# Kernel tuning notes

Measured on AMD Instinct MI355X. Metric: run time of the kernel, lower is better.

The kernel has to match this reference:

```python
import jax, jax.numpy as jnp
import numpy as np

B, N, C, H = 1, 2048, 1024, 16


def setup_inputs() -> dict:
    key = jax.random.key(0)
    ks = jax.random.split(key, 8)
    scale = 1.0 / np.sqrt(C)
    d = {"x": jax.random.normal(ks[0], (B, N, C), dtype=jnp.float32)}
    for i, name in enumerate(["q1", "q2", "k1", "k2", "v", "out"]):
        d[f"W_{name}"] = jax.random.normal(ks[1 + i], (C, C), dtype=jnp.float32) * scale
        d[f"b_{name}"] = jnp.zeros((C,), dtype=jnp.float32)
    d["ln_g"] = jnp.ones((C,), dtype=jnp.float32)
    d["ln_b"] = jnp.zeros((C,), dtype=jnp.float32)
    return d


def reference(x, W_q1, b_q1, W_q2, b_q2, W_k1, b_k1, W_k2, b_k2,
              W_v, b_v, W_out, b_out, ln_g, ln_b):
    Bx, Nx, Cx = x.shape
    hd = Cx // H  # head_dim

    def proj(W, b):
        # ResidualMLP with num_layers=-1 and in_dim==out_dim: x + Linear(x)
        return x + x @ W + b

    def split_heads(z):
        return z.reshape(Bx, Nx, H, hd).transpose(0, 2, 1, 3)  # b h n d

    # kernel='identity', norm_q=norm_k=False -> raw projections
    q1 = split_heads(proj(W_q1, b_q1))
    q2 = split_heads(proj(W_q2, b_q2))
    k1 = split_heads(proj(W_k1, b_k1))
    k2 = split_heads(proj(W_k2, b_k2))
    v = split_heads(proj(W_v, b_v))

    # triple attention: elementwise product of the two Gram matrices, then
    # row-normalized (flash-style softmax; kernel also returns lse which the
    # module discards: `_, out = self.attn(...)`)
    s = jnp.einsum('bhnd,bhmd->bhnm', q1, k1) * jnp.einsum('bhnd,bhmd->bhnm', q2, k2)
    p = jax.nn.softmax(s, axis=-1)
    o = jnp.einsum('bhnm,bhmd->bhnd', p, v)

    o = o.transpose(0, 2, 1, 3).reshape(Bx, Nx, Cx)  # b n (h d)

    # LayerNorm (eps=1e-5, torch default)
    mu = o.mean(axis=-1, keepdims=True)
    var = ((o - mu) ** 2).mean(axis=-1, keepdims=True)
    o = (o - mu) / jnp.sqrt(var + 1e-5) * ln_g + ln_b

    return o @ W_out + b_out
```

## Files before the change

### kernel.cpp

```cpp
#include <hip/hip_runtime.h>
#include <hip/hip_bf16.h>
#include <stdint.h>


#define N_SEQ 2048
#define CDIM  1024
#define NHEAD 16
#define HDIM  64

typedef __attribute__((ext_vector_type(8))) short bfrag;
typedef __attribute__((ext_vector_type(4))) float f4;
typedef __attribute__((ext_vector_type(16))) float f16v;
typedef unsigned short u16;

#define MFMA16(a, b, c) __builtin_amdgcn_mfma_f32_16x16x32_bf16((a), (b), (c), 0, 0, 0)
#define MFMA32(a, b, c) __builtin_amdgcn_mfma_f32_32x32x16_bf16((a), (b), (c), 0, 0, 0)

__device__ __forceinline__ float bf2f(u16 u) {
  union { unsigned int i; float f; } c; c.i = ((unsigned int)u) << 16; return c.f;
}
__device__ __forceinline__ u16 f2bf(float f) {
  union { float f; unsigned int i; } c; c.f = f;
  unsigned int i = c.i;
  return (u16)((i + 0x7FFFu + ((i >> 16) & 1u)) >> 16);
}
__device__ __forceinline__ unsigned int pk2(float lo, float hi) {
  __hip_bfloat162 b = __float22bfloat162_rn(make_float2(lo, hi));
  unsigned int u;
  __builtin_memcpy(&u, &b, 4);
  return u;
}

__device__ __forceinline__ void gld16(const void* g, void* lds) {
  __builtin_amdgcn_global_load_lds(
      (const __attribute__((address_space(1))) void*)g,
      (__attribute__((address_space(3))) void*)lds, 16, 0, 0);
}

__global__ __launch_bounds__(256) void k_split_x(
    const float* __restrict__ x, u16* __restrict__ xh, u16* __restrict__ xl) {
  int i = (blockIdx.x * 256 + threadIdx.x) * 4;
  float4 v = *(const float4*)(x + i);
  float vv[4] = {v.x, v.y, v.z, v.w};
  ushort4 h, l;
  u16 hh[4], ll[4];
#pragma unroll
  for (int j = 0; j < 4; j++) {
    hh[j] = f2bf(vv[j]);
    ll[j] = f2bf(vv[j] - bf2f(hh[j]));
  }
  h.x = hh[0]; h.y = hh[1]; h.z = hh[2]; h.w = hh[3];
  l.x = ll[0]; l.y = ll[1]; l.z = ll[2]; l.w = ll[3];
  *(ushort4*)(xh + i) = h;
  *(ushort4*)(xl + i) = l;
}

__global__ __launch_bounds__(256) void k_wsplit(
    const float* __restrict__ W0, const float* __restrict__ W1,
    const float* __restrict__ W2, const float* __restrict__ W3,
    const float* __restrict__ W4, const float* __restrict__ W5,
    u16* __restrict__ wth, u16* __restrict__ wtl) {
  __shared__ float tile[64][65];
  int wz = blockIdx.z;
  const float* W = wz == 0 ? W0 : wz == 1 ? W1 : wz == 2 ? W2 : wz == 3 ? W3 : wz == 4 ? W4 : W5;
  int kb = blockIdx.x * 64, nb = blockIdx.y * 64;
  int t = threadIdx.x;
  int r0 = t >> 4, c0 = (t & 15) * 4;
#pragma unroll
  for (int i = 0; i < 4; i++) {
    int r = r0 + i * 16;
    float4 v = *(const float4*)(W + (size_t)(kb + r) * CDIM + nb + c0);
    tile[r][c0 + 0] = v.x; tile[r][c0 + 1] = v.y; tile[r][c0 + 2] = v.z; tile[r][c0 + 3] = v.w;
  }
  __syncthreads();
#pragma unroll
  for (int i = 0; i < 4; i++) {
    int wn = (t >> 4) + i * 16;
    int wk = (t & 15) * 4;
    ushort4 h, l;
    u16 hh[4], ll[4];
#pragma unroll
    for (int j = 0; j < 4; j++) {
      float v = tile[wk + j][wn];
      hh[j] = f2bf(v);
      ll[j] = f2bf(v - bf2f(hh[j]));
    }
    h.x = hh[0]; h.y = hh[1]; h.z = hh[2]; h.w = hh[3];
    l.x = ll[0]; l.y = ll[1]; l.z = ll[2]; l.w = ll[3];
    size_t off = ((size_t)wz * CDIM + nb + wn) * CDIM + kb + wk;
    *(ushort4*)(wth + off) = h;
    if (wz < 4) *(ushort4*)(wtl + off) = l;
  }
}

__global__ __launch_bounds__(256, 2) void k_proj(
    const u16* __restrict__ xh, const u16* __restrict__ xl,
    const u16* __restrict__ wth, const u16* __restrict__ wtl,
    const float* __restrict__ x,
    const float* __restrict__ b0, const float* __restrict__ b1,
    const float* __restrict__ b2, const float* __restrict__ b3,
    const float* __restrict__ b4,
    u16* __restrict__ qh, u16* __restrict__ ql, u16* __restrict__ vT) {
  __shared__ u16 sAh[128 * 64];
  __shared__ u16 sAl[128 * 64];
  __shared__ u16 sBh[128 * 64];
  __shared__ u16 sBl[128 * 64];
  int t = threadIdx.x;
  int w = blockIdx.x >> 3;
  int n0 = (blockIdx.x & 7) * 128;
  int m0 = blockIdx.y * 128;
  int lane = t & 63, wid = t >> 6;
  int wm = (wid >> 1) * 64, wn = (wid & 1) * 64;
  int lr = lane & 15, lg = lane >> 4;
  const bool split = (w < 4);

  f4 acc[4][4];
#pragma unroll
  for (int i = 0; i < 4; i++)
#pragma unroll
    for (int j = 0; j < 4; j++) acc[i][j] = (f4)0.0f;

  const u16* wbh = wth + (size_t)w * CDIM * CDIM;
  const u16* wbl = wtl + (size_t)w * CDIM * CDIM;

  int srow = t >> 3;
  int scolsw = (((t & 7) ^ ((t >> 3) & 7)) * 8);
  int soff = srow * 64 + (t & 7) * 8;

  for (int kt = 0; kt < CDIM; kt += 64) {
#pragma unroll
    for (int c = 0; c < 4; c++) {
      gld16(xh + (size_t)(m0 + srow + c * 32) * CDIM + kt + scolsw, sAh + soff + c * 2048);
      gld16(wbh + (size_t)(n0 + srow + c * 32) * CDIM + kt + scolsw, sBh + soff + c * 2048);
      if (split) {
        gld16(xl + (size_t)(m0 + srow + c * 32) * CDIM + kt + scolsw, sAl + soff + c * 2048);
        gld16(wbl + (size_t)(n0 + srow + c * 32) * CDIM + kt + scolsw, sBl + soff + c * 2048);
      }
    }
    __syncthreads();
#pragma unroll
    for (int kk = 0; kk < 2; kk++) {
      int cc = (((kk * 4 + lg) ^ (lr & 7))) * 8;
      bfrag afh[4], bvh[4];
#pragma unroll
      for (int mi = 0; mi < 4; mi++)
        afh[mi] = *(const bfrag*)(sAh + (wm + mi * 16 + lr) * 64 + cc);
#pragma unroll
      for (int ni = 0; ni < 4; ni++)
        bvh[ni] = *(const bfrag*)(sBh + (wn + ni * 16 + lr) * 64 + cc);
#pragma unroll
      for (int mi = 0; mi < 4; mi++)
#pragma unroll
        for (int ni = 0; ni < 4; ni++)
          acc[mi][ni] = MFMA16(afh[mi], bvh[ni], acc[mi][ni]);
      if (split) {
        bfrag afl[4], bvl[4];
#pragma unroll
        for (int mi = 0; mi < 4; mi++)
          afl[mi] = *(const bfrag*)(sAl + (wm + mi * 16 + lr) * 64 + cc);
#pragma unroll
        for (int ni = 0; ni < 4; ni++)
          bvl[ni] = *(const bfrag*)(sBl + (wn + ni * 16 + lr) * 64 + cc);
#pragma unroll
        for (int mi = 0; mi < 4; mi++)
#pragma unroll
          for (int ni = 0; ni < 4; ni++) {
            acc[mi][ni] = MFMA16(afh[mi], bvl[ni], acc[mi][ni]);
            acc[mi][ni] = MFMA16(afl[mi], bvh[ni], acc[mi][ni]);
          }
      }
    }
    __syncthreads();
  }

  const float* bias = w == 0 ? b0 : w == 1 ? b1 : w == 2 ? b2 : w == 3 ? b3 : b4;
#pragma unroll
  for (int mi = 0; mi < 4; mi++) {
#pragma unroll
    for (int ni = 0; ni < 4; ni++) {
      int col = n0 + wn + ni * 16 + lr;
      int rowb = m0 + wm + mi * 16 + lg * 4;
      float vv[4];
#pragma unroll
      for (int r = 0; r < 4; r++)
        vv[r] = acc[mi][ni][r] + x[(size_t)(rowb + r) * CDIM + col] + bias[col];
      if (split) {
#pragma unroll
        for (int r = 0; r < 4; r++) {
          u16 h = f2bf(vv[r]);
          u16 l = f2bf(vv[r] - bf2f(h));
          qh[((size_t)w * N_SEQ + rowb + r) * CDIM + col] = h;
          ql[((size_t)w * N_SEQ + rowb + r) * CDIM + col] = l;
        }
      } else {
        ushort4 pv;
        pv.x = f2bf(vv[0]); pv.y = f2bf(vv[1]); pv.z = f2bf(vv[2]); pv.w = f2bf(vv[3]);
        *(ushort4*)(vT + (size_t)col * N_SEQ + rowb) = pv;
      }
    }
  }
}

__global__ __launch_bounds__(256, 2) void k_attn(
    const u16* __restrict__ qkh, const u16* __restrict__ qkl,
    const u16* __restrict__ vT, u16* __restrict__ O0, u16* __restrict__ O1,
    float2* __restrict__ ml) {
  __shared__ u16 sbuf[2][32 * 512];
  int bid = blockIdx.x;
  int khalf = bid >> 8;
  int inner = bid & 255;
  int vb = (inner & 7) * 32 + (inner >> 3);
  int h = vb >> 4;
  int qb = (vb & 15) * 128;
  int t = threadIdx.x, lane = t & 63, wv = t >> 6;
  int l31 = lane & 31, hi5 = lane >> 5;
  const size_t NC = (size_t)N_SEQ * CDIM;
  const int hoff = h * HDIM;
  const int k0 = khalf * (N_SEQ / 2);
  u16* Op = khalf ? O1 : O0;

  int qrow = qb + wv * 32 + l31;
  bfrag q1h[4], q1l[4], q2h[4], q2l[4];
#pragma unroll
  for (int ks = 0; ks < 4; ks++) {
    size_t off = (size_t)qrow * CDIM + hoff + ks * 16 + hi5 * 8;
    q1h[ks] = *(const bfrag*)(qkh + off);
    q1l[ks] = *(const bfrag*)(qkl + off);
    q2h[ks] = *(const bfrag*)(qkh + NC + off);
    q2l[ks] = *(const bfrag*)(qkl + NC + off);
  }

  const u16* kb = ((wv & 1) ? qkl : qkh) + (size_t)(2 + (wv >> 1)) * NC;

  float mrun = -1e30f, lrun = 0.f;
  f16v accO0 = (f16v)0.0f, accO1 = (f16v)0.0f;

#define STAGE(bi, kt)                                                          \
  {                                                                            \
    _Pragma("unroll") for (int i = 0; i < 8; i++) {                            \
      int kh_ = i >> 2, ksp_ = i & 3;                                          \
      gld16(kb + (size_t)((kt) + kh_ * 32 + l31) * CDIM + hoff + ksp_ * 16 +   \
                hi5 * 8,                                                       \
            sbuf[bi] + ((wv * 8 + i) << 9));                                   \
    }                                                                          \
  }

  STAGE(0, k0);
  asm volatile("s_waitcnt vmcnt(0)" ::: "memory");
  __builtin_amdgcn_s_barrier();

#pragma unroll 1
  for (int it = 0; it < N_SEQ / 2 / 64; it++) {
    int kt = k0 + it * 64;
    if (it + 1 < N_SEQ / 2 / 64) STAGE((it + 1) & 1, kt + 64);

    bfrag vld[2][4];
#pragma unroll
    for (int kh = 0; kh < 2; kh++) {
      const u16* vb0 = vT + (size_t)(hoff + l31) * N_SEQ + kt + kh * 32 + hi5 * 8;
      const u16* vb1 = vT + (size_t)(hoff + 32 + l31) * N_SEQ + kt + kh * 32 + hi5 * 8;
      vld[kh][0] = *(const bfrag*)(vb0);
      vld[kh][1] = *(const bfrag*)(vb0 + 16);
      vld[kh][2] = *(const bfrag*)(vb1);
      vld[kh][3] = *(const bfrag*)(vb1 + 16);
    }

    const u16* sb = sbuf[it & 1];
    f16v s1[2], s2[2];
#pragma unroll
    for (int kh = 0; kh < 2; kh++) { s1[kh] = (f16v)0.0f; s2[kh] = (f16v)0.0f; }
#pragma unroll
    for (int kh = 0; kh < 2; kh++) {
#pragma unroll
      for (int ks = 0; ks < 4; ks++) {
        const u16* cb = sb + ((kh * 4 + ks) << 9) + lane * 8;
        bfrag k1h = *(const bfrag*)(cb);
        bfrag k1l = *(const bfrag*)(cb + (8 << 9));
        bfrag k2h = *(const bfrag*)(cb + (16 << 9));
        bfrag k2l = *(const bfrag*)(cb + (24 << 9));
        s1[kh] = MFMA32(k1h, q1h[ks], s1[kh]);
        s1[kh] = MFMA32(k1h, q1l[ks], s1[kh]);
        s1[kh] = MFMA32(k1l, q1h[ks], s1[kh]);
        s2[kh] = MFMA32(k2h, q2h[ks], s2[kh]);
        s2[kh] = MFMA32(k2h, q2l[ks], s2[kh]);
        s2[kh] = MFMA32(k2l, q2h[ks], s2[kh]);
      }
    }
    f16v p0 = s1[0] * s2[0];
    f16v p1 = s1[1] * s2[1];

    float pm = fmaxf(p0[0], p1[0]);
#pragma unroll
    for (int j = 1; j < 16; j++) pm = fmaxf(pm, fmaxf(p0[j], p1[j]));
    pm = fmaxf(pm, __shfl_xor(pm, 32, 64));
    if (__any(pm > mrun + 8.0f)) {
      float mnew = fmaxf(mrun, pm);
      float sc = __expf(mrun - mnew);
      lrun *= sc;
#pragma unroll
      for (int j = 0; j < 16; j++) { accO0[j] *= sc; accO1[j] *= sc; }
      mrun = mnew;
    }
    float rs = 0.f;
#pragma unroll
    for (int j = 0; j < 16; j++) { p0[j] = __expf(p0[j] - mrun); rs += p0[j]; }
#pragma unroll
    for (int j = 0; j < 16; j++) { p1[j] = __expf(p1[j] - mrun); rs += p1[j]; }
    rs += __shfl_xor(rs, 32, 64);
    lrun += rs;

    unsigned dw[16];
#pragma unroll
    for (int j = 0; j < 8; j++) dw[j] = pk2(p0[2 * j], p0[2 * j + 1]);
#pragma unroll
    for (int j = 0; j < 8; j++) dw[8 + j] = pk2(p1[2 * j], p1[2 * j + 1]);

#pragma unroll
    for (int kh = 0; kh < 2; kh++) {
      unsigned j0 = dw[kh * 8 + 0], j1 = dw[kh * 8 + 1], j2 = dw[kh * 8 + 2],
               j3 = dw[kh * 8 + 3], j4 = dw[kh * 8 + 4], j5 = dw[kh * 8 + 5],
               j6 = dw[kh * 8 + 6], j7 = dw[kh * 8 + 7];
      unsigned pj0 = __shfl_xor(j0, 32, 64), pj1 = __shfl_xor(j1, 32, 64);
      unsigned pj2 = __shfl_xor(j2, 32, 64), pj3 = __shfl_xor(j3, 32, 64);
      unsigned pj4 = __shfl_xor(j4, 32, 64), pj5 = __shfl_xor(j5, 32, 64);
      unsigned pj6 = __shfl_xor(j6, 32, 64), pj7 = __shfl_xor(j7, 32, 64);
      union { unsigned u[4]; bfrag b; } f0, f1;
      f0.u[0] = hi5 ? pj2 : j0;
      f0.u[1] = hi5 ? pj3 : j1;
      f0.u[2] = hi5 ? j2 : pj0;
      f0.u[3] = hi5 ? j3 : pj1;
      f1.u[0] = hi5 ? pj6 : j4;
      f1.u[1] = hi5 ? pj7 : j5;
      f1.u[2] = hi5 ? j6 : pj4;
      f1.u[3] = hi5 ? j7 : pj5;
      accO0 = MFMA32(vld[kh][0], f0.b, accO0);
      accO0 = MFMA32(vld[kh][1], f1.b, accO0);
      accO1 = MFMA32(vld[kh][2], f0.b, accO1);
      accO1 = MFMA32(vld[kh][3], f1.b, accO1);
    }

    asm volatile("s_waitcnt vmcnt(0)" ::: "memory");
    __builtin_amdgcn_s_barrier();
  }
#undef STAGE

#pragma unroll
  for (int q4 = 0; q4 < 4; q4++) {
    ushort4 s0, s1v;
    s0.x = f2bf(accO0[q4 * 4 + 0]); s0.y = f2bf(accO0[q4 * 4 + 1]);
    s0.z = f2bf(accO0[q4 * 4 + 2]); s0.w = f2bf(accO0[q4 * 4 + 3]);
    s1v.x = f2bf(accO1[q4 * 4 + 0]); s1v.y = f2bf(accO1[q4 * 4 + 1]);
    s1v.z = f2bf(accO1[q4 * 4 + 2]); s1v.w = f2bf(accO1[q4 * 4 + 3]);
    *(ushort4*)(Op + (size_t)qrow * CDIM + hoff + q4 * 8 + hi5 * 4) = s0;
    *(ushort4*)(Op + (size_t)qrow * CDIM + hoff + 32 + q4 * 8 + hi5 * 4) = s1v;
  }
  if (!hi5) ml[(size_t)(khalf * NHEAD + h) * N_SEQ + qrow] = make_float2(mrun, lrun);
}

__global__ __launch_bounds__(256) void k_cln(
    const u16* __restrict__ O0, const u16* __restrict__ O1,
    const float2* __restrict__ ml, const float* __restrict__ g,
    const float* __restrict__ b, u16* __restrict__ oln) {
  __shared__ float rsm[4], rs2m[4];
  int row = blockIdx.x, t = threadIdx.x;
  int h = t >> 4;
  float2 a = ml[(size_t)h * N_SEQ + row];
  float2 bb = ml[(size_t)(NHEAD + h) * N_SEQ + row];
  float M = fmaxf(a.x, bb.x);
  float w0 = __expf(a.x - M), w1 = __expf(bb.x - M);
  float invL = 1.0f / (w0 * a.y + w1 * bb.y);
  ushort4 u0 = *(const ushort4*)(O0 + (size_t)row * CDIM + t * 4);
  ushort4 u1 = *(const ushort4*)(O1 + (size_t)row * CDIM + t * 4);
  float vals[4];
  vals[0] = (w0 * bf2f(u0.x) + w1 * bf2f(u1.x)) * invL;
  vals[1] = (w0 * bf2f(u0.y) + w1 * bf2f(u1.y)) * invL;
  vals[2] = (w0 * bf2f(u0.z) + w1 * bf2f(u1.z)) * invL;
  vals[3] = (w0 * bf2f(u0.w) + w1 * bf2f(u1.w)) * invL;
  float s = vals[0] + vals[1] + vals[2] + vals[3];
  float s2 = vals[0] * vals[0] + vals[1] * vals[1] + vals[2] * vals[2] + vals[3] * vals[3];
#pragma unroll
  for (int d = 1; d < 64; d <<= 1) {
    s += __shfl_xor(s, d, 64);
    s2 += __shfl_xor(s2, d, 64);
  }
  int wv = t >> 6;
  if ((t & 63) == 0) { rsm[wv] = s; rs2m[wv] = s2; }
  __syncthreads();
  s = rsm[0] + rsm[1] + rsm[2] + rsm[3];
  s2 = rs2m[0] + rs2m[1] + rs2m[2] + rs2m[3];
  float mu = s * (1.0f / CDIM);
  float var = s2 * (1.0f / CDIM) - mu * mu;
  float inv = rsqrtf(var + 1e-5f);
  ushort4 r4;
  u16 rr[4];
#pragma unroll
  for (int j = 0; j < 4; j++) {
    int col = t * 4 + j;
    rr[j] = f2bf((vals[j] - mu) * inv * g[col] + b[col]);
  }
  r4.x = rr[0]; r4.y = rr[1]; r4.z = rr[2]; r4.w = rr[3];
  *(ushort4*)(oln + (size_t)row * CDIM + t * 4) = r4;
}

__global__ __launch_bounds__(256, 2) void k_ogemm(
    const u16* __restrict__ A, const u16* __restrict__ Bw,
    const float* __restrict__ bias, float* __restrict__ out) {
  __shared__ u16 sA[128 * 64];
  __shared__ u16 sB[128 * 64];
  int t = threadIdx.x;
  int n0 = blockIdx.x * 128, m0 = blockIdx.y * 128;
  int lane = t & 63, wid = t >> 6;
  int wm = (wid >> 1) * 64, wn = (wid & 1) * 64;
  int lr = lane & 15, lg = lane >> 4;
  f4 acc[4][4];
#pragma unroll
  for (int i = 0; i < 4; i++)
#pragma unroll
    for (int j = 0; j < 4; j++) acc[i][j] = (f4)0.0f;
  int srow = t >> 3, scol = (t & 7) * 8, soff = srow * 64 + scol;
  for (int kt = 0; kt < CDIM; kt += 64) {
#pragma unroll
    for (int c = 0; c < 4; c++) {
      gld16(A + (size_t)(m0 + srow + c * 32) * CDIM + kt + scol, (u16*)sA + soff + c * 2048);
      gld16(Bw + (size_t)(n0 + srow + c * 32) * CDIM + kt + scol, (u16*)sB + soff + c * 2048);
    }
    __syncthreads();
#pragma unroll
    for (int kk = 0; kk < 2; kk++) {
      bfrag af[4], bv[4];
#pragma unroll
      for (int mi = 0; mi < 4; mi++)
        af[mi] = *(const bfrag*)(sA + (wm + mi * 16 + lr) * 64 + kk * 32 + lg * 8);
#pragma unroll
      for (int ni = 0; ni < 4; ni++)
        bv[ni] = *(const bfrag*)(sB + (wn + ni * 16 + lr) * 64 + kk * 32 + lg * 8);
#pragma unroll
      for (int mi = 0; mi < 4; mi++)
#pragma unroll
        for (int ni = 0; ni < 4; ni++)
          acc[mi][ni] = MFMA16(af[mi], bv[ni], acc[mi][ni]);
    }
    __syncthreads();
  }
#pragma unroll
  for (int mi = 0; mi < 4; mi++) {
#pragma unroll
    for (int ni = 0; ni < 4; ni++) {
      int col = n0 + wn + ni * 16 + lr;
      int rowb = m0 + wm + mi * 16 + lg * 4;
#pragma unroll
      for (int r = 0; r < 4; r++)
        out[(size_t)(rowb + r) * CDIM + col] = acc[mi][ni][r] + bias[col];
    }
  }
}

extern "C" void kernel_launch(void* const* d_in, const int* in_sizes, int n_in,
                              void* d_out, int out_size, void* d_ws, size_t ws_size,
                              hipStream_t stream) {
  const float* x   = (const float*)d_in[0];
  const float* Wq1 = (const float*)d_in[1];  const float* bq1 = (const float*)d_in[2];
  const float* Wq2 = (const float*)d_in[3];  const float* bq2 = (const float*)d_in[4];
  const float* Wk1 = (const float*)d_in[5];  const float* bk1 = (const float*)d_in[6];
  const float* Wk2 = (const float*)d_in[7];  const float* bk2 = (const float*)d_in[8];
  const float* Wv  = (const float*)d_in[9];  const float* bv  = (const float*)d_in[10];
  const float* Wo  = (const float*)d_in[11]; const float* bo  = (const float*)d_in[12];
  const float* lng = (const float*)d_in[13]; const float* lnb = (const float*)d_in[14];

  char* w = (char*)d_ws;
  u16* xh  = (u16*)(w + (0ull << 20));
  u16* xl  = (u16*)(w + (4ull << 20));
  u16* wth = (u16*)(w + (8ull << 20));
  u16* wtl = (u16*)(w + (20ull << 20));
  u16* qsh = (u16*)(w + (28ull << 20));
  u16* qsl = (u16*)(w + (44ull << 20));
  u16* vT  = (u16*)(w + (60ull << 20));
  u16* O0  = (u16*)(w + (0ull << 20));
  u16* O1  = (u16*)(w + (4ull << 20));
  float2* ml = (float2*)(w + (20ull << 20));
  u16* oln = (u16*)(w + (24ull << 20));

  k_split_x<<<2048, 256, 0, stream>>>(x, xh, xl);
  k_wsplit<<<dim3(16, 16, 6), 256, 0, stream>>>(Wq1, Wq2, Wk1, Wk2, Wv, Wo, wth, wtl);
  k_proj<<<dim3(40, 16), 256, 0, stream>>>(xh, xl, wth, wtl, x,
                                           bq1, bq2, bk1, bk2, bv, qsh, qsl, vT);
  k_attn<<<512, 256, 0, stream>>>(qsh, qsl, vT, O0, O1, ml);
  k_cln<<<2048, 256, 0, stream>>>(O0, O1, ml, lng, lnb, oln);
  k_ogemm<<<dim3(8, 16), 256, 0, stream>>>(oln, wth + 5ull * CDIM * CDIM, bo, (float*)d_out);
}
```

Baseline: 193.3 us.

## Split attention keys four ways with smaller tiles and higher occupancy

Splits the key dimension of the attention kernel into four partitions instead of two, doubling the grid to 1024 blocks. Each iteration now processes 32 keys instead of 64, which halves the shared-memory staging buffer and the register footprint so launch bounds can ask for 4 blocks per CU. It also raises wave priority around the QK MFMA section. The combine/LayerNorm kernel now merges four partial outputs with their max/sum statistics. Workspace buffers are relocated to fit the extra partials, at the cost of more partial-output traffic and more loop iterations with barriers.

```diff
diff --git a/kernel.cpp b/kernel.cpp
--- a/kernel.cpp
+++ b/kernel.cpp
@@ -201,13 +201,13 @@
   }
 }
 
-__global__ __launch_bounds__(256, 2) void k_attn(
+__global__ __launch_bounds__(256, 4) void k_attn(
     const u16* __restrict__ qkh, const u16* __restrict__ qkl,
     const u16* __restrict__ vT, u16* __restrict__ O0, u16* __restrict__ O1,
-    float2* __restrict__ ml) {
-  __shared__ u16 sbuf[2][32 * 512];
+    u16* __restrict__ O2, u16* __restrict__ O3, float2* __restrict__ ml) {
+  __shared__ u16 sbuf[2][16 * 512];
   int bid = blockIdx.x;
-  int khalf = bid >> 8;
+  int kq = bid >> 8;
   int inner = bid & 255;
   int vb = (inner & 7) * 32 + (inner >> 3);
   int h = vb >> 4;
@@ -216,8 +216,8 @@
   int l31 = lane & 31, hi5 = lane >> 5;
   const size_t NC = (size_t)N_SEQ * CDIM;
   const int hoff = h * HDIM;
-  const int k0 = khalf * (N_SEQ / 2);
-  u16* Op = khalf ? O1 : O0;
+  const int k0 = kq * (N_SEQ / 4);
+  u16* Op = kq == 0 ? O0 : kq == 1 ? O1 : kq == 2 ? O2 : O3;
 
   int qrow = qb + wv * 32 + l31;
   bfrag q1h[4], q1l[4], q2h[4], q2l[4];
@@ -237,11 +237,9 @@
 
 #define STAGE(bi, kt)                                                          \
   {                                                                            \
-    _Pragma("unroll") for (int i = 0; i < 8; i++) {                            \
-      int kh_ = i >> 2, ksp_ = i & 3;                                          \
-      gld16(kb + (size_t)((kt) + kh_ * 32 + l31) * CDIM + hoff + ksp_ * 16 +   \
-                hi5 * 8,                                                       \
-            sbuf[bi] + ((wv * 8 + i) << 9));                                   \
+    _Pragma("unroll") for (int i = 0; i < 4; i++) {                            \
+      gld16(kb + (size_t)((kt) + l31) * CDIM + hoff + i * 16 + hi5 * 8,        \
+            sbuf[bi] + ((wv * 4 + i) << 9));                                   \
     }                                                                          \
   }
 
@@ -250,48 +248,40 @@
   __builtin_amdgcn_s_barrier();
 
 #pragma unroll 1
-  for (int it = 0; it < N_SEQ / 2 / 64; it++) {
-    int kt = k0 + it * 64;
-    if (it + 1 < N_SEQ / 2 / 64) STAGE((it + 1) & 1, kt + 64);
-
-    bfrag vld[2][4];
-#pragma unroll
-    for (int kh = 0; kh < 2; kh++) {
-      const u16* vb0 = vT + (size_t)(hoff + l31) * N_SEQ + kt + kh * 32 + hi5 * 8;
-      const u16* vb1 = vT + (size_t)(hoff + 32 + l31) * N_SEQ + kt + kh * 32 + hi5 * 8;
-      vld[kh][0] = *(const bfrag*)(vb0);
-      vld[kh][1] = *(const bfrag*)(vb0 + 16);
-      vld[kh][2] = *(const bfrag*)(vb1);
-      vld[kh][3] = *(const bfrag*)(vb1 + 16);
-    }
+  for (int it = 0; it < N_SEQ / 4 / 32; it++) {
+    int kt = k0 + it * 32;
+    if (it + 1 < N_SEQ / 4 / 32) STAGE((it + 1) & 1, kt + 32);
+
+    const u16* vb0 = vT + (size_t)(hoff + l31) * N_SEQ + kt + hi5 * 8;
+    const u16* vb1 = vT + (size_t)(hoff + 32 + l31) * N_SEQ + kt + hi5 * 8;
+    bfrag vld0 = *(const bfrag*)(vb0);
+    bfrag vld1 = *(const bfrag*)(vb0 + 16);
+    bfrag vld2 = *(const bfrag*)(vb1);
+    bfrag vld3 = *(const bfrag*)(vb1 + 16);
 
     const u16* sb = sbuf[it & 1];
-    f16v s1[2], s2[2];
-#pragma unroll
-    for (int kh = 0; kh < 2; kh++) { s1[kh] = (f16v)0.0f; s2[kh] = (f16v)0.0f; }
-#pragma unroll
-    for (int kh = 0; kh < 2; kh++) {
-#pragma unroll
-      for (int ks = 0; ks < 4; ks++) {
-        const u16* cb = sb + ((kh * 4 + ks) << 9) + lane * 8;
-        bfrag k1h = *(const bfrag*)(cb);
-        bfrag k1l = *(const bfrag*)(cb + (8 << 9));
-        bfrag k2h = *(const bfrag*)(cb + (16 << 9));
-        bfrag k2l = *(const bfrag*)(cb + (24 << 9));
-        s1[kh] = MFMA32(k1h, q1h[ks], s1[kh]);
-        s1[kh] = MFMA32(k1h, q1l[ks], s1[kh]);
-        s1[kh] = MFMA32(k1l, q1h[ks], s1[kh]);
-        s2[kh] = MFMA32(k2h, q2h[ks], s2[kh]);
-        s2[kh] = MFMA32(k2h, q2l[ks], s2[kh]);
-        s2[kh] = MFMA32(k2l, q2h[ks], s2[kh]);
-      }
-    }
-    f16v p0 = s1[0] * s2[0];
-    f16v p1 = s1[1] * s2[1];
-
-    float pm = fmaxf(p0[0], p1[0]);
-#pragma unroll
-    for (int j = 1; j < 16; j++) pm = fmaxf(pm, fmaxf(p0[j], p1[j]));
+    f16v s1 = (f16v)0.0f, s2 = (f16v)0.0f;
+    __builtin_amdgcn_s_setprio(1);
+#pragma unroll
+    for (int ks = 0; ks < 4; ks++) {
+      const u16* cb = sb + (ks << 9) + lane * 8;
+      bfrag k1h = *(const bfrag*)(cb);
+      bfrag k1l = *(const bfrag*)(cb + (4 << 9));
+      bfrag k2h = *(const bfrag*)(cb + (8 << 9));
+      bfrag k2l = *(const bfrag*)(cb + (12 << 9));
+      s1 = MFMA32(k1h, q1h[ks], s1);
+      s1 = MFMA32(k1h, q1l[ks], s1);
+      s1 = MFMA32(k1l, q1h[ks], s1);
+      s2 = MFMA32(k2h, q2h[ks], s2);
+      s2 = MFMA32(k2h, q2l[ks], s2);
+      s2 = MFMA32(k2l, q2h[ks], s2);
+    }
+    __builtin_amdgcn_s_setprio(0);
+    f16v p = s1 * s2;
+
+    float pm = p[0];
+#pragma unroll
+    for (int j = 1; j < 16; j++) pm = fmaxf(pm, p[j]);
     pm = fmaxf(pm, __shfl_xor(pm, 32, 64));
     if (__any(pm > mrun + 8.0f)) {
       float mnew = fmaxf(mrun, pm);
@@ -303,41 +293,32 @@
     }
     float rs = 0.f;
 #pragma unroll
-    for (int j = 0; j < 16; j++) { p0[j] = __expf(p0[j] - mrun); rs += p0[j]; }
-#pragma unroll
-    for (int j = 0; j < 16; j++) { p1[j] = __expf(p1[j] - mrun); rs += p1[j]; }
+    for (int j = 0; j < 16; j++) { p[j] = __expf(p[j] - mrun); rs += p[j]; }
     rs += __shfl_xor(rs, 32, 64);
     lrun += rs;
 
-    unsigned dw[16];
-#pragma unroll
-    for (int j = 0; j < 8; j++) dw[j] = pk2(p0[2 * j], p0[2 * j + 1]);
-#pragma unroll
-    for (int j = 0; j < 8; j++) dw[8 + j] = pk2(p1[2 * j], p1[2 * j + 1]);
-
-#pragma unroll
-    for (int kh = 0; kh < 2; kh++) {
-      unsigned j0 = dw[kh * 8 + 0], j1 = dw[kh * 8 + 1], j2 = dw[kh * 8 + 2],
-               j3 = dw[kh * 8 + 3], j4 = dw[kh * 8 + 4], j5 = dw[kh * 8 + 5],
-               j6 = dw[kh * 8 + 6], j7 = dw[kh * 8 + 7];
-      unsigned pj0 = __shfl_xor(j0, 32, 64), pj1 = __shfl_xor(j1, 32, 64);
-      unsigned pj2 = __shfl_xor(j2, 32, 64), pj3 = __shfl_xor(j3, 32, 64);
-      unsigned pj4 = __shfl_xor(j4, 32, 64), pj5 = __shfl_xor(j5, 32, 64);
-      unsigned pj6 = __shfl_xor(j6, 32, 64), pj7 = __shfl_xor(j7, 32, 64);
-      union { unsigned u[4]; bfrag b; } f0, f1;
-      f0.u[0] = hi5 ? pj2 : j0;
-      f0.u[1] = hi5 ? pj3 : j1;
-      f0.u[2] = hi5 ? j2 : pj0;
-      f0.u[3] = hi5 ? j3 : pj1;
-      f1.u[0] = hi5 ? pj6 : j4;
-      f1.u[1] = hi5 ? pj7 : j5;
-      f1.u[2] = hi5 ? j6 : pj4;
-      f1.u[3] = hi5 ? j7 : pj5;
-      accO0 = MFMA32(vld[kh][0], f0.b, accO0);
-      accO0 = MFMA32(vld[kh][1], f1.b, accO0);
-      accO1 = MFMA32(vld[kh][2], f0.b, accO1);
-      accO1 = MFMA32(vld[kh][3], f1.b, accO1);
-    }
+    unsigned dw[8];
+#pragma unroll
+    for (int j = 0; j < 8; j++) dw[j] = pk2(p[2 * j], p[2 * j + 1]);
+    unsigned j0 = dw[0], j1 = dw[1], j2 = dw[2], j3 = dw[3],
+             j4 = dw[4], j5 = dw[5], j6 = dw[6], j7 = dw[7];
+    unsigned pj0 = __shfl_xor(j0, 32, 64), pj1 = __shfl_xor(j1, 32, 64);
+    unsigned pj2 = __shfl_xor(j2, 32, 64), pj3 = __shfl_xor(j3, 32, 64);
+    unsigned pj4 = __shfl_xor(j4, 32, 64), pj5 = __shfl_xor(j5, 32, 64);
+    unsigned pj6 = __shfl_xor(j6, 32, 64), pj7 = __shfl_xor(j7, 32, 64);
+    union { unsigned u[4]; bfrag b; } f0, f1;
+    f0.u[0] = hi5 ? pj2 : j0;
+    f0.u[1] = hi5 ? pj3 : j1;
+    f0.u[2] = hi5 ? j2 : pj0;
+    f0.u[3] = hi5 ? j3 : pj1;
+    f1.u[0] = hi5 ? pj6 : j4;
+    f1.u[1] = hi5 ? pj7 : j5;
+    f1.u[2] = hi5 ? j6 : pj4;
+    f1.u[3] = hi5 ? j7 : pj5;
+    accO0 = MFMA32(vld0, f0.b, accO0);
+    accO0 = MFMA32(vld1, f1.b, accO0);
+    accO1 = MFMA32(vld2, f0.b, accO1);
+    accO1 = MFMA32(vld3, f1.b, accO1);
 
     asm volatile("s_waitcnt vmcnt(0)" ::: "memory");
     __builtin_amdgcn_s_barrier();
@@ -354,28 +335,34 @@
     *(ushort4*)(Op + (size_t)qrow * CDIM + hoff + q4 * 8 + hi5 * 4) = s0;
     *(ushort4*)(Op + (size_t)qrow * CDIM + hoff + 32 + q4 * 8 + hi5 * 4) = s1v;
   }
-  if (!hi5) ml[(size_t)(khalf * NHEAD + h) * N_SEQ + qrow] = make_float2(mrun, lrun);
+  if (!hi5) ml[(size_t)(kq * NHEAD + h) * N_SEQ + qrow] = make_float2(mrun, lrun);
 }
 
 __global__ __launch_bounds__(256) void k_cln(
     const u16* __restrict__ O0, const u16* __restrict__ O1,
+    const u16* __restrict__ O2, const u16* __restrict__ O3,
     const float2* __restrict__ ml, const float* __restrict__ g,
     const float* __restrict__ b, u16* __restrict__ oln) {
   __shared__ float rsm[4], rs2m[4];
   int row = blockIdx.x, t = threadIdx.x;
   int h = t >> 4;
-  float2 a = ml[(size_t)h * N_SEQ + row];
-  float2 bb = ml[(size_t)(NHEAD + h) * N_SEQ + row];
-  float M = fmaxf(a.x, bb.x);
-  float w0 = __expf(a.x - M), w1 = __expf(bb.x - M);
-  float invL = 1.0f / (w0 * a.y + w1 * bb.y);
+  float2 a0 = ml[(size_t)(0 * NHEAD + h) * N_SEQ + row];
+  float2 a1 = ml[(size_t)(1 * NHEAD + h) * N_SEQ + row];
+  float2 a2 = ml[(size_t)(2 * NHEAD + h) * N_SEQ + row];
+  float2 a3 = ml[(size_t)(3 * NHEAD + h) * N_SEQ + row];
+  float M = fmaxf(fmaxf(a0.x, a1.x), fmaxf(a2.x, a3.x));
+  float w0 = __expf(a0.x - M), w1 = __expf(a1.x - M);
+  float w2 = __expf(a2.x - M), w3 = __expf(a3.x - M);
+  float invL = 1.0f / (w0 * a0.y + w1 * a1.y + w2 * a2.y + w3 * a3.y);
   ushort4 u0 = *(const ushort4*)(O0 + (size_t)row * CDIM + t * 4);
   ushort4 u1 = *(const ushort4*)(O1 + (size_t)row * CDIM + t * 4);
+  ushort4 u2 = *(const ushort4*)(O2 + (size_t)row * CDIM + t * 4);
+  ushort4 u3 = *(const ushort4*)(O3 + (size_t)row * CDIM + t * 4);
   float vals[4];
-  vals[0] = (w0 * bf2f(u0.x) + w1 * bf2f(u1.x)) * invL;
-  vals[1] = (w0 * bf2f(u0.y) + w1 * bf2f(u1.y)) * invL;
-  vals[2] = (w0 * bf2f(u0.z) + w1 * bf2f(u1.z)) * invL;
-  vals[3] = (w0 * bf2f(u0.w) + w1 * bf2f(u1.w)) * invL;
+  vals[0] = (w0 * bf2f(u0.x) + w1 * bf2f(u1.x) + w2 * bf2f(u2.x) + w3 * bf2f(u3.x)) * invL;
+  vals[1] = (w0 * bf2f(u0.y) + w1 * bf2f(u1.y) + w2 * bf2f(u2.y) + w3 * bf2f(u3.y)) * invL;
+  vals[2] = (w0 * bf2f(u0.z) + w1 * bf2f(u1.z) + w2 * bf2f(u2.z) + w3 * bf2f(u3.z)) * invL;
+  vals[3] = (w0 * bf2f(u0.w) + w1 * bf2f(u1.w) + w2 * bf2f(u2.w) + w3 * bf2f(u3.w)) * invL;
   float s = vals[0] + vals[1] + vals[2] + vals[3];
   float s2 = vals[0] * vals[0] + vals[1] * vals[1] + vals[2] * vals[2] + vals[3] * vals[3];
 #pragma unroll
@@ -477,14 +464,16 @@
   u16* vT  = (u16*)(w + (60ull << 20));
   u16* O0  = (u16*)(w + (0ull << 20));
   u16* O1  = (u16*)(w + (4ull << 20));
-  float2* ml = (float2*)(w + (20ull << 20));
-  u16* oln = (u16*)(w + (24ull << 20));
+  u16* O2  = (u16*)(w + (20ull << 20));
+  u16* O3  = (u16*)(w + (24ull << 20));
+  float2* ml = (float2*)(w + (8ull << 20));
+  u16* oln = (u16*)(w + (28ull << 20));
 
   k_split_x<<<2048, 256, 0, stream>>>(x, xh, xl);
   k_wsplit<<<dim3(16, 16, 6), 256, 0, stream>>>(Wq1, Wq2, Wk1, Wk2, Wv, Wo, wth, wtl);
   k_proj<<<dim3(40, 16), 256, 0, stream>>>(xh, xl, wth, wtl, x,
                                            bq1, bq2, bk1, bk2, bv, qsh, qsl, vT);
-  k_attn<<<512, 256, 0, stream>>>(qsh, qsl, vT, O0, O1, ml);
-  k_cln<<<2048, 256, 0, stream>>>(O0, O1, ml, lng, lnb, oln);
+  k_attn<<<1024, 256, 0, stream>>>(qsh, qsl, vT, O0, O1, O2, O3, ml);
+  k_cln<<<2048, 256, 0, stream>>>(O0, O1, O2, O3, ml, lng, lnb, oln);
   k_ogemm<<<dim3(8, 16), 256, 0, stream>>>(oln, wth + 5ull * CDIM * CDIM, bo, (float*)d_out);
 }
```

Measured after the change: 269.2 us. 1.39x slower.

## Software-pipeline QK MFMA with softmax/PV across key half-tiles

Applied to the files above, without the earlier changes.

Splits each 64-key tile into two 32-key halves and interleaves the QK score MFMAs of one half with the softmax and PV work of the other, so matrix ops can overlap the exp/shuffle work. The next tile's first half is computed right after the barrier, and the global-to-LDS staging moves two tiles ahead, issued after the barrier. This adds live registers for the second set of score accumulators and makes the buffer reuse and barrier ordering harder to reason about.

```diff
diff --git a/kernel.cpp b/kernel.cpp
--- a/kernel.cpp
+++ b/kernel.cpp
@@ -245,104 +245,98 @@
     }                                                                          \
   }
 
+#define QKH(S1, S2, sb_, kh)                                                   \
+  {                                                                            \
+    S1 = (f16v)0.0f; S2 = (f16v)0.0f;                                          \
+    _Pragma("unroll") for (int ks = 0; ks < 4; ks++) {                         \
+      const u16* cb = (sb_) + (((kh) * 4 + ks) << 9) + lane * 8;               \
+      bfrag k1h_ = *(const bfrag*)(cb);                                        \
+      bfrag k1l_ = *(const bfrag*)(cb + (8 << 9));                             \
+      bfrag k2h_ = *(const bfrag*)(cb + (16 << 9));                            \
+      bfrag k2l_ = *(const bfrag*)(cb + (24 << 9));                            \
+      S1 = MFMA32(k1h_, q1h[ks], S1);                                          \
+      S1 = MFMA32(k1h_, q1l[ks], S1);                                          \
+      S1 = MFMA32(k1l_, q1h[ks], S1);                                          \
+      S2 = MFMA32(k2h_, q2h[ks], S2);                                          \
+      S2 = MFMA32(k2h_, q2l[ks], S2);                                          \
+      S2 = MFMA32(k2l_, q2h[ks], S2);                                          \
+    }                                                                          \
+  }
+
+#define SMPV(S1, S2, kt_, kh)                                                  \
+  {                                                                            \
+    const u16* vb0 = vT + (size_t)(hoff + l31) * N_SEQ + (kt_) + (kh) * 32 + hi5 * 8; \
+    const u16* vb1 = vT + (size_t)(hoff + 32 + l31) * N_SEQ + (kt_) + (kh) * 32 + hi5 * 8; \
+    bfrag vld0 = *(const bfrag*)(vb0);                                         \
+    bfrag vld1 = *(const bfrag*)(vb0 + 16);                                    \
+    bfrag vld2 = *(const bfrag*)(vb1);                                         \
+    bfrag vld3 = *(const bfrag*)(vb1 + 16);                                    \
+    f16v p = (S1) * (S2);                                                      \
+    float pm = p[0];                                                           \
+    _Pragma("unroll") for (int j = 1; j < 16; j++) pm = fmaxf(pm, p[j]);       \
+    pm = fmaxf(pm, __shfl_xor(pm, 32, 64));                                    \
+    if (__any(pm > mrun + 8.0f)) {                                             \
+      float mnew = fmaxf(mrun, pm);                                            \
+      float sc = __expf(mrun - mnew);                                          \
+      lrun *= sc;                                                              \
+      _Pragma("unroll") for (int j = 0; j < 16; j++) {                         \
+        accO0[j] *= sc; accO1[j] *= sc;                                        \
+      }                                                                        \
+      mrun = mnew;                                                             \
+    }                                                                          \
+    float rs = 0.f;                                                            \
+    _Pragma("unroll") for (int j = 0; j < 16; j++) {                           \
+      p[j] = __expf(p[j] - mrun);                                              \
+      rs += p[j];                                                              \
+    }                                                                          \
+    rs += __shfl_xor(rs, 32, 64);                                              \
+    lrun += rs;                                                                \
+    unsigned dw[8];                                                            \
+    _Pragma("unroll") for (int j = 0; j < 8; j++) dw[j] = pk2(p[2 * j], p[2 * j + 1]); \
+    unsigned j0 = dw[0], j1 = dw[1], j2 = dw[2], j3 = dw[3],                   \
+             j4 = dw[4], j5 = dw[5], j6 = dw[6], j7 = dw[7];                   \
+    unsigned pj0 = __shfl_xor(j0, 32, 64), pj1 = __shfl_xor(j1, 32, 64);       \
+    unsigned pj2 = __shfl_xor(j2, 32, 64), pj3 = __shfl_xor(j3, 32, 64);       \
+    unsigned pj4 = __shfl_xor(j4, 32, 64), pj5 = __shfl_xor(j5, 32, 64);       \
+    unsigned pj6 = __shfl_xor(j6, 32, 64), pj7 = __shfl_xor(j7, 32, 64);       \
+    union { unsigned u[4]; bfrag b; } f0, f1;                                  \
+    f0.u[0] = hi5 ? pj2 : j0;                                                  \
+    f0.u[1] = hi5 ? pj3 : j1;                                                  \
+    f0.u[2] = hi5 ? j2 : pj0;                                                  \
+    f0.u[3] = hi5 ? j3 : pj1;                                                  \
+    f1.u[0] = hi5 ? pj6 : j4;                                                  \
+    f1.u[1] = hi5 ? pj7 : j5;                                                  \
+    f1.u[2] = hi5 ? j6 : pj4;                                                  \
+    f1.u[3] = hi5 ? j7 : pj5;                                                  \
+    accO0 = MFMA32(vld0, f0.b, accO0);                                         \
+    accO0 = MFMA32(vld1, f1.b, accO0);                                         \
+    accO1 = MFMA32(vld2, f0.b, accO1);                                         \
+    accO1 = MFMA32(vld3, f1.b, accO1);                                         \
+  }
+
   STAGE(0, k0);
   asm volatile("s_waitcnt vmcnt(0)" ::: "memory");
   __builtin_amdgcn_s_barrier();
+  STAGE(1, k0 + 64);
+
+  f16v a1, a2, b1, b2;
+  QKH(a1, a2, &sbuf[0][0], 0);
 
 #pragma unroll 1
   for (int it = 0; it < N_SEQ / 2 / 64; it++) {
     int kt = k0 + it * 64;
-    if (it + 1 < N_SEQ / 2 / 64) STAGE((it + 1) & 1, kt + 64);
-
-    bfrag vld[2][4];
-#pragma unroll
-    for (int kh = 0; kh < 2; kh++) {
-      const u16* vb0 = vT + (size_t)(hoff + l31) * N_SEQ + kt + kh * 32 + hi5 * 8;
-      const u16* vb1 = vT + (size_t)(hoff + 32 + l31) * N_SEQ + kt + kh * 32 + hi5 * 8;
-      vld[kh][0] = *(const bfrag*)(vb0);
-      vld[kh][1] = *(const bfrag*)(vb0 + 16);
-      vld[kh][2] = *(const bfrag*)(vb1);
-      vld[kh][3] = *(const bfrag*)(vb1 + 16);
-    }
-
-    const u16* sb = sbuf[it & 1];
-    f16v s1[2], s2[2];
-#pragma unroll
-    for (int kh = 0; kh < 2; kh++) { s1[kh] = (f16v)0.0f; s2[kh] = (f16v)0.0f; }
-#pragma unroll
-    for (int kh = 0; kh < 2; kh++) {
-#pragma unroll
-      for (int ks = 0; ks < 4; ks++) {
-        const u16* cb = sb + ((kh * 4 + ks) << 9) + lane * 8;
-        bfrag k1h = *(const bfrag*)(cb);
-        bfrag k1l = *(const bfrag*)(cb + (8 << 9));
-        bfrag k2h = *(const bfrag*)(cb + (16 << 9));
-        bfrag k2l = *(const bfrag*)(cb + (24 << 9));
-        s1[kh] = MFMA32(k1h, q1h[ks], s1[kh]);
-        s1[kh] = MFMA32(k1h, q1l[ks], s1[kh]);
-        s1[kh] = MFMA32(k1l, q1h[ks], s1[kh]);
-        s2[kh] = MFMA32(k2h, q2h[ks], s2[kh]);
-        s2[kh] = MFMA32(k2h, q2l[ks], s2[kh]);
-        s2[kh] = MFMA32(k2l, q2h[ks], s2[kh]);
-      }
-    }
-    f16v p0 = s1[0] * s2[0];
-    f16v p1 = s1[1] * s2[1];
-
-    float pm = fmaxf(p0[0], p1[0]);
-#pragma unroll
-    for (int j = 1; j < 16; j++) pm = fmaxf(pm, fmaxf(p0[j], p1[j]));
-    pm = fmaxf(pm, __shfl_xor(pm, 32, 64));
-    if (__any(pm > mrun + 8.0f)) {
-      float mnew = fmaxf(mrun, pm);
-      float sc = __expf(mrun - mnew);
-      lrun *= sc;
-#pragma unroll
-      for (int j = 0; j < 16; j++) { accO0[j] *= sc; accO1[j] *= sc; }
-      mrun = mnew;
-    }
-    float rs = 0.f;
-#pragma unroll
-    for (int j = 0; j < 16; j++) { p0[j] = __expf(p0[j] - mrun); rs += p0[j]; }
-#pragma unroll
-    for (int j = 0; j < 16; j++) { p1[j] = __expf(p1[j] - mrun); rs += p1[j]; }
-    rs += __shfl_xor(rs, 32, 64);
-    lrun += rs;
-
-    unsigned dw[16];
-#pragma unroll
-    for (int j = 0; j < 8; j++) dw[j] = pk2(p0[2 * j], p0[2 * j + 1]);
-#pragma unroll
-    for (int j = 0; j < 8; j++) dw[8 + j] = pk2(p1[2 * j], p1[2 * j + 1]);
-
-#pragma unroll
-    for (int kh = 0; kh < 2; kh++) {
-      unsigned j0 = dw[kh * 8 + 0], j1 = dw[kh * 8 + 1], j2 = dw[kh * 8 + 2],
-               j3 = dw[kh * 8 + 3], j4 = dw[kh * 8 + 4], j5 = dw[kh * 8 + 5],
-               j6 = dw[kh * 8 + 6], j7 = dw[kh * 8 + 7];
-      unsigned pj0 = __shfl_xor(j0, 32, 64), pj1 = __shfl_xor(j1, 32, 64);
-      unsigned pj2 = __shfl_xor(j2, 32, 64), pj3 = __shfl_xor(j3, 32, 64);
-      unsigned pj4 = __shfl_xor(j4, 32, 64), pj5 = __shfl_xor(j5, 32, 64);
-      unsigned pj6 = __shfl_xor(j6, 32, 64), pj7 = __shfl_xor(j7, 32, 64);
-      union { unsigned u[4]; bfrag b; } f0, f1;
-      f0.u[0] = hi5 ? pj2 : j0;
-      f0.u[1] = hi5 ? pj3 : j1;
-      f0.u[2] = hi5 ? j2 : pj0;
-      f0.u[3] = hi5 ? j3 : pj1;
-      f1.u[0] = hi5 ? pj6 : j4;
-      f1.u[1] = hi5 ? pj7 : j5;
-      f1.u[2] = hi5 ? j6 : pj4;
-      f1.u[3] = hi5 ? j7 : pj5;
-      accO0 = MFMA32(vld[kh][0], f0.b, accO0);
-      accO0 = MFMA32(vld[kh][1], f1.b, accO0);
-      accO1 = MFMA32(vld[kh][2], f0.b, accO1);
-      accO1 = MFMA32(vld[kh][3], f1.b, accO1);
-    }
-
+    const u16* sbc = &sbuf[it & 1][0];
+    QKH(b1, b2, sbc, 1);
+    SMPV(a1, a2, kt, 0);
     asm volatile("s_waitcnt vmcnt(0)" ::: "memory");
     __builtin_amdgcn_s_barrier();
+    if (it + 2 < N_SEQ / 2 / 64) STAGE(it & 1, kt + 128);
+    if (it + 1 < N_SEQ / 2 / 64) QKH(a1, a2, &sbuf[(it + 1) & 1][0], 0);
+    SMPV(b1, b2, kt, 1);
   }
 #undef STAGE
+#undef QKH
+#undef SMPV
 
 #pragma unroll
   for (int q4 = 0; q4 < 4; q4++) {
```

Result: no change. 194.4 us (+0.6%).

## Rewrite attention kernel with 16x16 MFMA tiles, smaller blocks, swizzled LDS

Applied to the files above, without the earlier changes.

Rewrites the attention kernel around 16x16x32 MFMA instead of 32x32x16. Each block now covers 64 query rows over 32-key tiles, so the grid doubles to 1024 blocks and launch bounds target 4 blocks per SM. K tiles are staged into an XOR-swizzled LDS buffer to avoid bank conflicts. The double-buffered prefetch is dropped in favour of single-buffer load, wait and barrier each iteration, which trades latency hiding for occupancy and a smaller register and LDS footprint. Smaller MFMA tiles also mean more instructions per FLOP and more barriers.

```diff
diff --git a/kernel.cpp b/kernel.cpp
--- a/kernel.cpp
+++ b/kernel.cpp
@@ -10,11 +10,9 @@
 
 typedef __attribute__((ext_vector_type(8))) short bfrag;
 typedef __attribute__((ext_vector_type(4))) float f4;
-typedef __attribute__((ext_vector_type(16))) float f16v;
 typedef unsigned short u16;
 
 #define MFMA16(a, b, c) __builtin_amdgcn_mfma_f32_16x16x32_bf16((a), (b), (c), 0, 0, 0)
-#define MFMA32(a, b, c) __builtin_amdgcn_mfma_f32_32x32x16_bf16((a), (b), (c), 0, 0, 0)
 
 __device__ __forceinline__ float bf2f(u16 u) {
   union { unsigned int i; float f; } c; c.i = ((unsigned int)u) << 16; return c.f;
@@ -201,29 +199,29 @@
   }
 }
 
-__global__ __launch_bounds__(256, 2) void k_attn(
+__global__ __launch_bounds__(256, 4) void k_attn(
     const u16* __restrict__ qkh, const u16* __restrict__ qkl,
     const u16* __restrict__ vT, u16* __restrict__ O0, u16* __restrict__ O1,
     float2* __restrict__ ml) {
-  __shared__ u16 sbuf[2][32 * 512];
+  __shared__ u16 sbuf[8192];
   int bid = blockIdx.x;
-  int khalf = bid >> 8;
-  int inner = bid & 255;
-  int vb = (inner & 7) * 32 + (inner >> 3);
-  int h = vb >> 4;
-  int qb = (vb & 15) * 128;
+  int khalf = bid >> 9;
+  int inner = bid & 511;
+  int vb = (inner & 7) * 64 + (inner >> 3);
+  int h = vb >> 5;
+  int qb = (vb & 31) * 64;
   int t = threadIdx.x, lane = t & 63, wv = t >> 6;
-  int l31 = lane & 31, hi5 = lane >> 5;
+  int lq = lane & 15, lg = lane >> 4;
   const size_t NC = (size_t)N_SEQ * CDIM;
   const int hoff = h * HDIM;
   const int k0 = khalf * (N_SEQ / 2);
   u16* Op = khalf ? O1 : O0;
 
-  int qrow = qb + wv * 32 + l31;
-  bfrag q1h[4], q1l[4], q2h[4], q2l[4];
-#pragma unroll
-  for (int ks = 0; ks < 4; ks++) {
-    size_t off = (size_t)qrow * CDIM + hoff + ks * 16 + hi5 * 8;
+  int qrow = qb + wv * 16 + lq;
+  bfrag q1h[2], q1l[2], q2h[2], q2l[2];
+#pragma unroll
+  for (int ks = 0; ks < 2; ks++) {
+    size_t off = (size_t)qrow * CDIM + hoff + ks * 32 + lg * 8;
     q1h[ks] = *(const bfrag*)(qkh + off);
     q1l[ks] = *(const bfrag*)(qkl + off);
     q2h[ks] = *(const bfrag*)(qkh + NC + off);
@@ -231,130 +229,112 @@
   }
 
   const u16* kb = ((wv & 1) ? qkl : qkh) + (size_t)(2 + (wv >> 1)) * NC;
+  const int swsrc = ((lane & 7) ^ (lane >> 3)) * 8;
 
   float mrun = -1e30f, lrun = 0.f;
-  f16v accO0 = (f16v)0.0f, accO1 = (f16v)0.0f;
-
-#define STAGE(bi, kt)                                                          \
+  f4 accO[4];
+#pragma unroll
+  for (int d = 0; d < 4; d++) accO[d] = (f4)0.0f;
+
+#define STAGE(kt)                                                              \
   {                                                                            \
-    _Pragma("unroll") for (int i = 0; i < 8; i++) {                            \
-      int kh_ = i >> 2, ksp_ = i & 3;                                          \
-      gld16(kb + (size_t)((kt) + kh_ * 32 + l31) * CDIM + hoff + ksp_ * 16 +   \
-                hi5 * 8,                                                       \
-            sbuf[bi] + ((wv * 8 + i) << 9));                                   \
+    _Pragma("unroll") for (int i = 0; i < 4; i++) {                            \
+      int ksub_ = i >> 1, hh_ = i & 1;                                         \
+      gld16(kb + (size_t)((kt) + ksub_ * 16 + hh_ * 8 + (lane >> 3)) * CDIM +  \
+                hoff + swsrc,                                                  \
+            sbuf + (wv * 2 + ksub_) * 1024 + hh_ * 512 + lane * 8);            \
     }                                                                          \
   }
 
-  STAGE(0, k0);
-  asm volatile("s_waitcnt vmcnt(0)" ::: "memory");
-  __builtin_amdgcn_s_barrier();
-
 #pragma unroll 1
-  for (int it = 0; it < N_SEQ / 2 / 64; it++) {
-    int kt = k0 + it * 64;
-    if (it + 1 < N_SEQ / 2 / 64) STAGE((it + 1) & 1, kt + 64);
-
-    bfrag vld[2][4];
-#pragma unroll
-    for (int kh = 0; kh < 2; kh++) {
-      const u16* vb0 = vT + (size_t)(hoff + l31) * N_SEQ + kt + kh * 32 + hi5 * 8;
-      const u16* vb1 = vT + (size_t)(hoff + 32 + l31) * N_SEQ + kt + kh * 32 + hi5 * 8;
-      vld[kh][0] = *(const bfrag*)(vb0);
-      vld[kh][1] = *(const bfrag*)(vb0 + 16);
-      vld[kh][2] = *(const bfrag*)(vb1);
-      vld[kh][3] = *(const bfrag*)(vb1 + 16);
-    }
-
-    const u16* sb = sbuf[it & 1];
-    f16v s1[2], s2[2];
-#pragma unroll
-    for (int kh = 0; kh < 2; kh++) { s1[kh] = (f16v)0.0f; s2[kh] = (f16v)0.0f; }
-#pragma unroll
-    for (int kh = 0; kh < 2; kh++) {
-#pragma unroll
-      for (int ks = 0; ks < 4; ks++) {
-        const u16* cb = sb + ((kh * 4 + ks) << 9) + lane * 8;
-        bfrag k1h = *(const bfrag*)(cb);
-        bfrag k1l = *(const bfrag*)(cb + (8 << 9));
-        bfrag k2h = *(const bfrag*)(cb + (16 << 9));
-        bfrag k2l = *(const bfrag*)(cb + (24 << 9));
-        s1[kh] = MFMA32(k1h, q1h[ks], s1[kh]);
-        s1[kh] = MFMA32(k1h, q1l[ks], s1[kh]);
-        s1[kh] = MFMA32(k1l, q1h[ks], s1[kh]);
-        s2[kh] = MFMA32(k2h, q2h[ks], s2[kh]);
-        s2[kh] = MFMA32(k2h, q2l[ks], s2[kh]);
-        s2[kh] = MFMA32(k2l, q2h[ks], s2[kh]);
+  for (int it = 0; it < N_SEQ / 2 / 32; it++) {
+    int kt = k0 + it * 32;
+    __builtin_amdgcn_s_barrier();
+    STAGE(kt);
+    asm volatile("s_waitcnt vmcnt(0)" ::: "memory");
+    __builtin_amdgcn_s_barrier();
+
+    f4 s1[2], s2[2];
+#pragma unroll
+    for (int ksub = 0; ksub < 2; ksub++) { s1[ksub] = (f4)0.0f; s2[ksub] = (f4)0.0f; }
+#pragma unroll
+    for (int ksub = 0; ksub < 2; ksub++) {
+#pragma unroll
+      for (int ks = 0; ks < 2; ks++) {
+        int ro = ksub * 1024 + lq * 64 + (((ks * 4 + lg) ^ (lq & 7)) * 8);
+        bfrag k1h_ = *(const bfrag*)(sbuf + ro);
+        bfrag k1l_ = *(const bfrag*)(sbuf + 2048 + ro);
+        bfrag k2h_ = *(const bfrag*)(sbuf + 4096 + ro);
+        bfrag k2l_ = *(const bfrag*)(sbuf + 6144 + ro);
+        s1[ksub] = MFMA16(k1h_, q1h[ks], s1[ksub]);
+        s1[ksub] = MFMA16(k1h_, q1l[ks], s1[ksub]);
+        s1[ksub] = MFMA16(k1l_, q1h[ks], s1[ksub]);
+        s2[ksub] = MFMA16(k2h_, q2h[ks], s2[ksub]);
+        s2[ksub] = MFMA16(k2h_, q2l[ks], s2[ksub]);
+        s2[ksub] = MFMA16(k2l_, q2h[ks], s2[ksub]);
       }
     }
-    f16v p0 = s1[0] * s2[0];
-    f16v p1 = s1[1] * s2[1];
-
-    float pm = fmaxf(p0[0], p1[0]);
-#pragma unroll
-    for (int j = 1; j < 16; j++) pm = fmaxf(pm, fmaxf(p0[j], p1[j]));
+
+    bfrag vf[4];
+#pragma unroll
+    for (int dt = 0; dt < 4; dt++)
+      vf[dt] = *(const bfrag*)(vT + (size_t)(hoff + dt * 16 + lq) * N_SEQ + kt + lg * 8);
+
+    f4 p0 = s1[0] * s2[0];
+    f4 p1 = s1[1] * s2[1];
+
+    float pm = fmaxf(fmaxf(fmaxf(p0[0], p0[1]), fmaxf(p0[2], p0[3])),
+                     fmaxf(fmaxf(p1[0], p1[1]), fmaxf(p1[2], p1[3])));
+    pm = fmaxf(pm, __shfl_xor(pm, 16, 64));
     pm = fmaxf(pm, __shfl_xor(pm, 32, 64));
     if (__any(pm > mrun + 8.0f)) {
       float mnew = fmaxf(mrun, pm);
       float sc = __expf(mrun - mnew);
       lrun *= sc;
 #pragma unroll
-      for (int j = 0; j < 16; j++) { accO0[j] *= sc; accO1[j] *= sc; }
+      for (int dt = 0; dt < 4; dt++)
+#pragma unroll
+        for (int j = 0; j < 4; j++) accO[dt][j] *= sc;
       mrun = mnew;
     }
     float rs = 0.f;
 #pragma unroll
-    for (int j = 0; j < 16; j++) { p0[j] = __expf(p0[j] - mrun); rs += p0[j]; }
-#pragma unroll
-    for (int j = 0; j < 16; j++) { p1[j] = __expf(p1[j] - mrun); rs += p1[j]; }
+    for (int j = 0; j < 4; j++) { p0[j] = __expf(p0[j] - mrun); rs += p0[j]; }
+#pragma unroll
+    for (int j = 0; j < 4; j++) { p1[j] = __expf(p1[j] - mrun); rs += p1[j]; }
+    rs += __shfl_xor(rs, 16, 64);
     rs += __shfl_xor(rs, 32, 64);
     lrun += rs;
 
-    unsigned dw[16];
-#pragma unroll
-    for (int j = 0; j < 8; j++) dw[j] = pk2(p0[2 * j], p0[2 * j + 1]);
-#pragma unroll
-    for (int j = 0; j < 8; j++) dw[8 + j] = pk2(p1[2 * j], p1[2 * j + 1]);
-
-#pragma unroll
-    for (int kh = 0; kh < 2; kh++) {
-      unsigned j0 = dw[kh * 8 + 0], j1 = dw[kh * 8 + 1], j2 = dw[kh * 8 + 2],
-               j3 = dw[kh * 8 + 3], j4 = dw[kh * 8 + 4], j5 = dw[kh * 8 + 5],
-               j6 = dw[kh * 8 + 6], j7 = dw[kh * 8 + 7];
-      unsigned pj0 = __shfl_xor(j0, 32, 64), pj1 = __shfl_xor(j1, 32, 64);
-      unsigned pj2 = __shfl_xor(j2, 32, 64), pj3 = __shfl_xor(j3, 32, 64);
-      unsigned pj4 = __shfl_xor(j4, 32, 64), pj5 = __shfl_xor(j5, 32, 64);
-      unsigned pj6 = __shfl_xor(j6, 32, 64), pj7 = __shfl_xor(j7, 32, 64);
-      union { unsigned u[4]; bfrag b; } f0, f1;
-      f0.u[0] = hi5 ? pj2 : j0;
-      f0.u[1] = hi5 ? pj3 : j1;
-      f0.u[2] = hi5 ? j2 : pj0;
-      f0.u[3] = hi5 ? j3 : pj1;
-      f1.u[0] = hi5 ? pj6 : j4;
-      f1.u[1] = hi5 ? pj7 : j5;
-      f1.u[2] = hi5 ? j6 : pj4;
-      f1.u[3] = hi5 ? j7 : pj5;
-      accO0 = MFMA32(vld[kh][0], f0.b, accO0);
-      accO0 = MFMA32(vld[kh][1], f1.b, accO0);
-      accO1 = MFMA32(vld[kh][2], f0.b, accO1);
-      accO1 = MFMA32(vld[kh][3], f1.b, accO1);
-    }
-
-    asm volatile("s_waitcnt vmcnt(0)" ::: "memory");
-    __builtin_amdgcn_s_barrier();
+    unsigned dws0 = pk2(p0[0], p0[1]), dws1 = pk2(p0[2], p0[3]);
+    unsigned dws2 = pk2(p1[0], p1[1]), dws3 = pk2(p1[2], p1[3]);
+    int srcA = ((lg & 1) * 2) * 16 + lq;
+    int srcB = srcA + 16;
+    unsigned a00 = __shfl(dws0, srcA, 64), a01 = __shfl(dws1, srcA, 64);
+    unsigned b00 = __shfl(dws0, srcB, 64), b01 = __shfl(dws1, srcB, 64);
+    unsigned a10 = __shfl(dws2, srcA, 64), a11 = __shfl(dws3, srcA, 64);
+    unsigned b10 = __shfl(dws2, srcB, 64), b11 = __shfl(dws3, srcB, 64);
+    int sel = lg >> 1;
+    union { unsigned u[4]; bfrag b; } pf;
+    pf.u[0] = sel ? a10 : a00;
+    pf.u[1] = sel ? a11 : a01;
+    pf.u[2] = sel ? b10 : b00;
+    pf.u[3] = sel ? b11 : b01;
+
+#pragma unroll
+    for (int dt = 0; dt < 4; dt++)
+      accO[dt] = MFMA16(vf[dt], pf.b, accO[dt]);
   }
 #undef STAGE
 
 #pragma unroll
-  for (int q4 = 0; q4 < 4; q4++) {
-    ushort4 s0, s1v;
-    s0.x = f2bf(accO0[q4 * 4 + 0]); s0.y = f2bf(accO0[q4 * 4 + 1]);
-    s0.z = f2bf(accO0[q4 * 4 + 2]); s0.w = f2bf(accO0[q4 * 4 + 3]);
-    s1v.x = f2bf(accO1[q4 * 4 + 0]); s1v.y = f2bf(accO1[q4 * 4 + 1]);
-    s1v.z = f2bf(accO1[q4 * 4 + 2]); s1v.w = f2bf(accO1[q4 * 4 + 3]);
-    *(ushort4*)(Op + (size_t)qrow * CDIM + hoff + q4 * 8 + hi5 * 4) = s0;
-    *(ushort4*)(Op + (size_t)qrow * CDIM + hoff + 32 + q4 * 8 + hi5 * 4) = s1v;
-  }
-  if (!hi5) ml[(size_t)(khalf * NHEAD + h) * N_SEQ + qrow] = make_float2(mrun, lrun);
+  for (int dt = 0; dt < 4; dt++) {
+    ushort4 sv;
+    sv.x = f2bf(accO[dt][0]); sv.y = f2bf(accO[dt][1]);
+    sv.z = f2bf(accO[dt][2]); sv.w = f2bf(accO[dt][3]);
+    *(ushort4*)(Op + (size_t)qrow * CDIM + hoff + dt * 16 + lg * 4) = sv;
+  }
+  if (lg == 0) ml[(size_t)(khalf * NHEAD + h) * N_SEQ + qrow] = make_float2(mrun, lrun);
 }
 
 __global__ __launch_bounds__(256) void k_cln(
@@ -484,7 +464,7 @@
   k_wsplit<<<dim3(16, 16, 6), 256, 0, stream>>>(Wq1, Wq2, Wk1, Wk2, Wv, Wo, wth, wtl);
   k_proj<<<dim3(40, 16), 256, 0, stream>>>(xh, xl, wth, wtl, x,
                                            bq1, bq2, bk1, bk2, bv, qsh, qsl, vT);
-  k_attn<<<512, 256, 0, stream>>>(qsh, qsl, vT, O0, O1, ml);
+  k_attn<<<1024, 256, 0, stream>>>(qsh, qsl, vT, O0, O1, ml);
   k_cln<<<2048, 256, 0, stream>>>(O0, O1, ml, lng, lnb, oln);
   k_ogemm<<<dim3(8, 16), 256, 0, stream>>>(oln, wth + 5ull * CDIM * CDIM, bo, (float*)d_out);
 }
```

After: 205.3 us. +6.2%, slower.
